# Optimization experiments

Measured on AMD Instinct MI355X. Metric: run time of the kernel, lower is better.

The kernel has to match this reference:

```python
import jax, jax.numpy as jnp
import numpy as np

NUM_GAUSSIANS = 20
NUM_LETTERS = 80
HIDDEN_SIZE = 400
ATTENTION_SCALE = 0.05
B, U = 1024, 1024


def setup_inputs() -> dict:
    key = jax.random.key(0)
    k1, k2, k3, k4, k5 = jax.random.split(key, 5)
    text_inputs = jax.random.randint(k1, (B, U), 0, NUM_LETTERS)          # [B, U] int
    text_lengths = jax.random.randint(k2, (B,), 0, U)                     # [B] int
    y_0 = jax.random.normal(k3, (B, HIDDEN_SIZE), dtype=jnp.float32)      # [B, H]
    prev_k = jax.random.uniform(k4, (B, NUM_GAUSSIANS), dtype=jnp.float32)  # [B, N]
    # window_layer params: Linear(H, 3N)
    kw, kb = jax.random.split(k5)
    lim = 1.0 / np.sqrt(HIDDEN_SIZE)
    W = jax.random.uniform(kw, (3 * NUM_GAUSSIANS, HIDDEN_SIZE), minval=-lim, maxval=lim, dtype=jnp.float32)
    bias = jax.random.uniform(kb, (3 * NUM_GAUSSIANS,), minval=-lim, maxval=lim, dtype=jnp.float32)
    return {"text_inputs": text_inputs, "text_lengths": text_lengths,
            "y_0": y_0, "prev_k": prev_k, "W": W, "bias": bias}


def reference(text_inputs, text_lengths, y_0, prev_k, W, bias):
    N = prev_k.shape[1]
    batch, maxlen = text_inputs.shape
    out = y_0 @ W.T + bias                                   # [B, 3N]
    a = jnp.exp(out[:, :N])[..., None]                       # [B, N, 1]
    b = jnp.exp(out[:, N:2 * N])[..., None]                  # [B, N, 1]
    k = (jnp.exp(out[:, 2 * N:]) * ATTENTION_SCALE + prev_k)[..., None]  # [B, N, 1]
    u = jnp.arange(maxlen, dtype=out.dtype)[None, None, :]   # [1, 1, U]
    text_mask = (jnp.arange(maxlen)[None, :] < text_lengths[:, None]).astype(out.dtype)  # [B, U]
    phi_t_u = jnp.sum(a * jnp.exp(-b * (k - u) ** 2), axis=1) * text_mask  # [B, U]
    # w_t = sum_u one_hot(text)[b,u,:] * phi[b,u]  ==  scatter-add over letter dim
    rows = jnp.arange(batch)[:, None]                        # [B, 1]
    w_t = jnp.zeros((batch, NUM_LETTERS), dtype=out.dtype).at[rows, text_inputs].add(phi_t_u)  # [B, L]
    return (w_t, k[..., 0], phi_t_u)
```

## Files before the change

### kernel.cpp

```cpp
#include <hip/hip_runtime.h>

#define NG 20
#define NL 80
#define HS 400
#define ASCALE 0.05f
#define BB 1024
#define UU 1024
#define LOG2E 1.4426950408889634f

__global__ __launch_bounds__(256) void window_fused_kernel(
    const int*   __restrict__ text,
    const int*   __restrict__ tlen,
    const float* __restrict__ y0,
    const float* __restrict__ prevk,
    const float* __restrict__ W,
    const float* __restrict__ bias,
    float* __restrict__ w_t,
    float* __restrict__ k_out,
    float* __restrict__ phi_out)
{
    const int b   = blockIdx.x;
    const int tid = threadIdx.x;

    __shared__ float yrow[HS];
    __shared__ float LAs[NG], B2s[NG], Ks[NG];
    __shared__ float wloc[NL];

    if (tid < HS / 4) {
        reinterpret_cast<float4*>(yrow)[tid] =
            reinterpret_cast<const float4*>(y0 + b * HS)[tid];
    }
    if (tid < NL) wloc[tid] = 0.f;
    __syncthreads();

    if (tid < 3 * NG * 4) {
        const int j = tid >> 2;
        const int p = tid & 3;
        const float4* wr = reinterpret_cast<const float4*>(W + j * HS + p * 100);
        const float4* yr = reinterpret_cast<const float4*>(yrow + p * 100);
        float s = 0.f;
        #pragma unroll 5
        for (int i = 0; i < 25; ++i) {
            const float4 w4 = wr[i];
            const float4 y4 = yr[i];
            s += w4.x * y4.x + w4.y * y4.y + w4.z * y4.z + w4.w * y4.w;
        }
        s += __shfl_down(s, 1, 4);
        s += __shfl_down(s, 2, 4);
        if (p == 0) {
            const float val = s + bias[j];
            if (j < NG) {
                LAs[j] = val * LOG2E;
            } else if (j < 2 * NG) {
                B2s[j - NG] = __expf(val) * LOG2E;
            } else {
                const int g = j - 2 * NG;
                const float kk = __expf(val) * ASCALE + prevk[b * NG + g];
                Ks[g] = kk;
                k_out[b * NG + g] = kk;
            }
        }
    }
    __syncthreads();

    float la[NG], b2[NG], kg[NG];
    #pragma unroll
    for (int n = 0; n < NG; ++n) { la[n] = LAs[n]; b2[n] = B2s[n]; kg[n] = Ks[n]; }

    const int len = tlen[b];
    #pragma unroll
    for (int ui = 0; ui < UU / 256; ++ui) {
        const int u = ui * 256 + tid;
        const int letter = text[b * UU + u];
        float s = 0.f;
        if (u < len) {
            const float uf = (float)u;
            #pragma unroll
            for (int n = 0; n < NG; ++n) {
                const float d = kg[n] - uf;
                s += exp2f(__builtin_fmaf(-b2[n] * d, d, la[n]));
            }
        }
        phi_out[b * UU + u] = s;
        if (s != 0.f) {
            atomicAdd(&wloc[letter], s);
        }
    }
    __syncthreads();

    if (tid < NL) w_t[b * NL + tid] = wloc[tid];
}

extern "C" void kernel_launch(void* const* d_in, const int* in_sizes, int n_in,
                              void* d_out, int out_size, void* d_ws, size_t ws_size,
                              hipStream_t stream) {
    const int*   text  = (const int*)  d_in[0];
    const int*   tlen  = (const int*)  d_in[1];
    const float* y0    = (const float*)d_in[2];
    const float* prevk = (const float*)d_in[3];
    const float* W     = (const float*)d_in[4];
    const float* bias  = (const float*)d_in[5];

    float* out   = (float*)d_out;
    float* w_t   = out;
    float* k_out = out + BB * NL;
    float* phi   = out + BB * NL + BB * NG;

    hipLaunchKernelGGL(window_fused_kernel, dim3(BB), dim3(256), 0, stream,
                       text, tlen, y0, prevk, W, bias, w_t, k_out, phi);
}
```

Measured before the change: 76.48 us.

## Process four contiguous positions per thread with vectorized loads/stores and raw exp2

Each thread now handles four adjacent sequence positions, so text is read as one int4 and phi is written as one float4. The text and length loads are hoisted to kernel start so their latency overlaps the GEMV phase. Exp2 uses the raw hardware builtin, and launch bounds now request four blocks per CU. This cuts the number of memory transactions and the instruction overhead. The trade-off is strided rather than coalesced per-instruction access and a masking change for tail positions.

```diff
diff --git a/kernel.cpp b/kernel.cpp
--- a/kernel.cpp
+++ b/kernel.cpp
@@ -8,7 +8,7 @@
 #define UU 1024
 #define LOG2E 1.4426950408889634f
 
-__global__ __launch_bounds__(256) void window_fused_kernel(
+__global__ __launch_bounds__(256, 4) void window_fused_kernel(
     const int*   __restrict__ text,
     const int*   __restrict__ tlen,
     const float* __restrict__ y0,
@@ -21,6 +21,9 @@
 {
     const int b   = blockIdx.x;
     const int tid = threadIdx.x;
+
+    const int4 letters = reinterpret_cast<const int4*>(text + b * UU)[tid];
+    const int  len     = tlen[b];
 
     __shared__ float yrow[HS];
     __shared__ float LAs[NG], B2s[NG], Ks[NG];
@@ -67,25 +70,32 @@
     #pragma unroll
     for (int n = 0; n < NG; ++n) { la[n] = LAs[n]; b2[n] = B2s[n]; kg[n] = Ks[n]; }
 
-    const int len = tlen[b];
-    #pragma unroll
-    for (int ui = 0; ui < UU / 256; ++ui) {
-        const int u = ui * 256 + tid;
-        const int letter = text[b * UU + u];
-        float s = 0.f;
-        if (u < len) {
-            const float uf = (float)u;
-            #pragma unroll
-            for (int n = 0; n < NG; ++n) {
-                const float d = kg[n] - uf;
-                s += exp2f(__builtin_fmaf(-b2[n] * d, d, la[n]));
-            }
+    const int u0 = tid * 4;
+    float s0 = 0.f, s1 = 0.f, s2 = 0.f, s3 = 0.f;
+    if (u0 < len) {
+        const float uf = (float)u0;
+        #pragma unroll
+        for (int n = 0; n < NG; ++n) {
+            const float d0 = kg[n] - uf;
+            const float d1 = d0 - 1.f;
+            const float d2 = d0 - 2.f;
+            const float d3 = d0 - 3.f;
+            s0 += __builtin_amdgcn_exp2f(__builtin_fmaf(-b2[n] * d0, d0, la[n]));
+            s1 += __builtin_amdgcn_exp2f(__builtin_fmaf(-b2[n] * d1, d1, la[n]));
+            s2 += __builtin_amdgcn_exp2f(__builtin_fmaf(-b2[n] * d2, d2, la[n]));
+            s3 += __builtin_amdgcn_exp2f(__builtin_fmaf(-b2[n] * d3, d3, la[n]));
         }
-        phi_out[b * UU + u] = s;
-        if (s != 0.f) {
-            atomicAdd(&wloc[letter], s);
-        }
+        if (u0 + 1 >= len) s1 = 0.f;
+        if (u0 + 2 >= len) s2 = 0.f;
+        if (u0 + 3 >= len) s3 = 0.f;
     }
+    float4 phi4; phi4.x = s0; phi4.y = s1; phi4.z = s2; phi4.w = s3;
+    reinterpret_cast<float4*>(phi_out + b * UU)[tid] = phi4;
+
+    if (s0 != 0.f) atomicAdd(&wloc[letters.x], s0);
+    if (s1 != 0.f) atomicAdd(&wloc[letters.y], s1);
+    if (s2 != 0.f) atomicAdd(&wloc[letters.z], s2);
+    if (s3 != 0.f) atomicAdd(&wloc[letters.w], s3);
     __syncthreads();
 
     if (tid < NL) w_t[b * NL + tid] = wloc[tid];
```

Result: no change. 75.69 us (-1.0%).
